# Performance work log

Hardware: AMD Instinct MI355X
Metric: run time of the kernel (lower is better)

Reference implementation:

```python
import jax, jax.numpy as jnp
import numpy as np

N = 1_000_000   # active voxels
C_IN = 32
C_OUT = 32
K = 27          # 3x3x3 kernel volume


def setup_inputs() -> dict:
    key = jax.random.key(0)
    k1, k2, k3, k4, k5 = jax.random.split(key, 5)
    in_feature = jax.random.normal(k1, (N, C_IN), dtype=jnp.float32)
    # torch init: uniform(-std, std), std = 1/sqrt(in_channels * kernel_volume)
    std = 1.0 / np.sqrt(C_IN * K)
    weight = jax.random.uniform(k2, (K, C_IN, C_OUT), jnp.float32, -std, std)
    bias = jax.random.uniform(k3, (C_OUT,), jnp.float32, -std, std)
    # kernel map: for each kernel offset k and each output voxel n, the index of
    # the contributing input voxel, plus a validity mask (sparse neighborhoods)
    kmap_idx = jax.random.randint(k4, (K, N), 0, N, dtype=jnp.int32)
    kmap_valid = jax.random.randint(k5, (K, N), 0, 2, dtype=jnp.int32).astype(bool)
    # center tap of a stride-1 sparse conv always maps voxel to itself
    kmap_idx = kmap_idx.at[K // 2].set(jnp.arange(N, dtype=jnp.int32))
    kmap_valid = kmap_valid.at[K // 2].set(True)
    return {
        "in_feature": in_feature,
        "weight": weight,
        "bias": bias,
        "kmap_idx": kmap_idx,
        "kmap_valid": kmap_valid,
    }


def reference(in_feature, weight, bias, kmap_idx, kmap_valid):
    # Gather-GEMM-scatter sparse conv: out[n] = sum_k W[k]^T @ x[kmap[k,n]] (if valid) + b
    # Loop over the 27 kernel taps (fixed kernel volume) to avoid materializing
    # the full [N, 27, C_in] gathered tensor.
    n_out = kmap_idx.shape[1]
    out = jnp.zeros((n_out, weight.shape[2]), dtype=in_feature.dtype)
    for k in range(weight.shape[0]):
        g = in_feature[kmap_idx[k]] * kmap_valid[k][:, None].astype(in_feature.dtype)
        out = out + jnp.einsum("nc,cd->nd", g, weight[k])
    return out + bias
```

## Files before the change

kernel.cpp:

```cpp
#include <hip/hip_runtime.h>
#include <stdint.h>

#define KVOL 27
#define CIN  32
#define COUT 32

typedef short bf16x8 __attribute__((ext_vector_type(8)));
typedef float f32x4  __attribute__((ext_vector_type(4)));

__global__ void detect_valid_layout(const uint8_t* __restrict__ valid_bytes,
                                    int* __restrict__ flag) {
    __shared__ int s_sum;
    if (threadIdx.x == 0) s_sum = 0;
    __syncthreads();
    int local = 0;
    for (int g = threadIdx.x; g < 1024; g += 256) {
        local += valid_bytes[4 * g + 1] + valid_bytes[4 * g + 2] + valid_bytes[4 * g + 3];
    }
    atomicAdd(&s_sum, local);
    __syncthreads();
    if (threadIdx.x == 0) flag[0] = (s_sum == 0) ? 1 : 0;
}

__device__ inline unsigned short f2bf(float f) {
    unsigned int u = __float_as_uint(f);
    return (unsigned short)((u + 0x7fffu + ((u >> 16) & 1u)) >> 16);
}

__global__ __launch_bounds__(256)
void convert_x(const float* __restrict__ X, short* __restrict__ Xb, int n8) {
    int i = blockIdx.x * blockDim.x + threadIdx.x;
    if (i >= n8) return;
    const float4* p = (const float4*)X + 2 * (size_t)i;
    float4 f0 = p[0], f1 = p[1];
    bf16x8 o;
    o[0] = (short)f2bf(f0.x); o[1] = (short)f2bf(f0.y);
    o[2] = (short)f2bf(f0.z); o[3] = (short)f2bf(f0.w);
    o[4] = (short)f2bf(f1.x); o[5] = (short)f2bf(f1.y);
    o[6] = (short)f2bf(f1.z); o[7] = (short)f2bf(f1.w);
    *((bf16x8*)Xb + (size_t)i) = o;
}

__global__ __launch_bounds__(256)
void convert_w(const float* __restrict__ W, short* __restrict__ Wt) {
    int i = blockIdx.x * blockDim.x + threadIdx.x;
    if (i >= KVOL * CIN * COUT) return;
    int k  = i >> 10;
    int co = (i >> 5) & 31;
    int ci = i & 31;
    Wt[i] = (short)f2bf(W[k * 1024 + ci * 32 + co]);
}

__global__ __launch_bounds__(256)
void sparse_conv_mfma(const short* __restrict__ Xb,
                      const short* __restrict__ Wt,
                      const float* __restrict__ bias,
                      const int* __restrict__ idx,
                      const uint8_t* __restrict__ validb,
                      const int* __restrict__ flag,
                      float* __restrict__ out, int N) {
    const int lane = threadIdx.x & 63;
    const int wave = threadIdx.x >> 6;
    const int col  = lane & 15;
    const int quad = lane >> 4;
    const int base = blockIdx.x * 256 + wave * 64;

    const bool int_layout = (flag[0] != 0);
    const int* validi = (const int*)validb;

    f32x4 acc[4][2] = {};
    const bf16x8 zero = {};

    for (int k = 0; k < KVOL; ++k) {
        const size_t koff = (size_t)k * (size_t)N;
        const bf16x8 b0 = *(const bf16x8*)(Wt + ((k * 32 + col)      * 32 + quad * 8));
        const bf16x8 b1 = *(const bf16x8*)(Wt + ((k * 32 + col + 16) * 32 + quad * 8));
        bf16x8 a[4];
#pragma unroll
        for (int g = 0; g < 4; ++g) {
            const int r = base + g * 16 + col;
            bool v = false;
            int  j = 0;
            if (r < N) {
                v = int_layout ? (validi[koff + r] != 0) : (validb[koff + r] != 0);
                j = idx[koff + r];
            }
            if (v) a[g] = *(const bf16x8*)(Xb + (size_t)j * CIN + quad * 8);
            else   a[g] = zero;
        }
#pragma unroll
        for (int g = 0; g < 4; ++g) {
            acc[g][0] = __builtin_amdgcn_mfma_f32_16x16x32_bf16(a[g], b0, acc[g][0], 0, 0, 0);
            acc[g][1] = __builtin_amdgcn_mfma_f32_16x16x32_bf16(a[g], b1, acc[g][1], 0, 0, 0);
        }
    }

    const float bv0 = bias[col];
    const float bv1 = bias[col + 16];
#pragma unroll
    for (int g = 0; g < 4; ++g) {
#pragma unroll
        for (int r = 0; r < 4; ++r) {
            const int row = base + g * 16 + quad * 4 + r;
            if (row < N) {
                out[(size_t)row * COUT + col]      = acc[g][0][r] + bv0;
                out[(size_t)row * COUT + col + 16] = acc[g][1][r] + bv1;
            }
        }
    }
}

__global__ __launch_bounds__(256)
void sparse_conv_fp32(const float* __restrict__ X,
                      const float* __restrict__ W,
                      const float* __restrict__ B,
                      const int* __restrict__ idx,
                      const uint8_t* __restrict__ validb,
                      const int* __restrict__ flag,
                      float* __restrict__ out,
                      int N) {
    const int n = blockIdx.x * blockDim.x + threadIdx.x;
    if (n >= N) return;
    const bool int_layout = (flag[0] != 0);
    const int* validi = (const int*)validb;
    float acc[COUT];
#pragma unroll
    for (int co = 0; co < COUT; ++co) acc[co] = B[co];
    for (int k = 0; k < KVOL; ++k) {
        const size_t kn = (size_t)k * (size_t)N + (size_t)n;
        const int v = int_layout ? validi[kn] : (int)validb[kn];
        if (v) {
            const int j = idx[kn];
            const float4* xp = (const float4*)(X + (size_t)j * CIN);
            float xr[CIN];
#pragma unroll
            for (int q = 0; q < 8; ++q) {
                float4 t = xp[q];
                xr[4 * q + 0] = t.x; xr[4 * q + 1] = t.y;
                xr[4 * q + 2] = t.z; xr[4 * q + 3] = t.w;
            }
            const float* __restrict__ Wk = W + k * CIN * COUT;
#pragma unroll
            for (int ci = 0; ci < CIN; ++ci) {
                const float xv = xr[ci];
#pragma unroll
                for (int co = 0; co < COUT; ++co) acc[co] += xv * Wk[ci * COUT + co];
            }
        }
    }
    float4* op = (float4*)(out + (size_t)n * COUT);
#pragma unroll
    for (int q = 0; q < 8; ++q)
        op[q] = make_float4(acc[4 * q + 0], acc[4 * q + 1], acc[4 * q + 2], acc[4 * q + 3]);
}

extern "C" void kernel_launch(void* const* d_in, const int* in_sizes, int n_in,
                              void* d_out, int out_size, void* d_ws, size_t ws_size,
                              hipStream_t stream) {
    const float*   X      = (const float*)d_in[0];
    const float*   W      = (const float*)d_in[1];
    const float*   B      = (const float*)d_in[2];
    const int*     idx    = (const int*)d_in[3];
    const uint8_t* validb = (const uint8_t*)d_in[4];

    const int N = in_sizes[0] / CIN;

    const size_t xb_bytes = (size_t)N * CIN * sizeof(short);
    const size_t wt_bytes = (size_t)KVOL * CIN * COUT * sizeof(short);
    const size_t need     = xb_bytes + wt_bytes + 256;

    if (ws_size >= need) {
        short* Xb  = (short*)d_ws;
        short* Wt  = (short*)((char*)d_ws + xb_bytes);
        int*   flag = (int*)((char*)d_ws + xb_bytes + wt_bytes);

        detect_valid_layout<<<1, 256, 0, stream>>>(validb, flag);

        const int n8 = (N * CIN) / 8;
        convert_x<<<(n8 + 255) / 256, 256, 0, stream>>>(X, Xb, n8);
        convert_w<<<(KVOL * CIN * COUT + 255) / 256, 256, 0, stream>>>(W, Wt);

        const int blocks = (N + 255) / 256;
        sparse_conv_mfma<<<blocks, 256, 0, stream>>>(Xb, Wt, B, idx, validb,
                                                     flag, (float*)d_out, N);
    } else {
        int* flag = (int*)d_ws;
        detect_valid_layout<<<1, 256, 0, stream>>>(validb, flag);
        const int blocks = (N + 255) / 256;
        sparse_conv_fp32<<<blocks, 256, 0, stream>>>(X, W, B, idx, validb,
                                                     flag, (float*)d_out, N);
    }
}
```

Measured before the change: 686.2 us.

## Preload kernel map into LDS, use zero sentinel row, double-buffer gathers

Each wave now loads all 27 index/valid pairs for its 64 rows up front in batches of nine, folds validity into the index by pointing invalid entries at an appended zero row of the bf16 feature buffer, and stores the result in shared memory. The tap loop reads indices from LDS and gathers branch-free, alternating two register sets so the next tap's gather is issued before the current tap's MFMAs. This is meant to hide gather latency and remove per-tap scattered index/valid loads and branches. It costs about 27 KB of LDS per block, which may limit occupancy, plus one extra 64-byte row in the workspace.

```diff
diff --git a/kernel.cpp b/kernel.cpp
--- a/kernel.cpp
+++ b/kernel.cpp
@@ -30,6 +30,10 @@
 __global__ __launch_bounds__(256)
 void convert_x(const float* __restrict__ X, short* __restrict__ Xb, int n8) {
     int i = blockIdx.x * blockDim.x + threadIdx.x;
+    if (i < 4) {
+        bf16x8 z = {};
+        *((bf16x8*)Xb + (size_t)n8 + i) = z;
+    }
     if (i >= n8) return;
     const float4* p = (const float4*)X + 2 * (size_t)i;
     float4 f0 = p[0], f1 = p[1];
@@ -65,46 +69,83 @@
     const int quad = lane >> 4;
     const int base = blockIdx.x * 256 + wave * 64;
 
+    __shared__ int s_idx[4][KVOL * 64];
+    int* sw = &s_idx[wave][0];
+
     const bool int_layout = (flag[0] != 0);
     const int* validi = (const int*)validb;
 
+    const int r = base + lane;
+    if (r < N) {
+        if (int_layout) {
+#pragma unroll
+            for (int kc = 0; kc < KVOL; kc += 9) {
+                int j[9], v[9];
+#pragma unroll
+                for (int t = 0; t < 9; ++t) j[t] = idx[(size_t)(kc + t) * N + r];
+#pragma unroll
+                for (int t = 0; t < 9; ++t) v[t] = validi[(size_t)(kc + t) * N + r];
+#pragma unroll
+                for (int t = 0; t < 9; ++t) sw[(kc + t) * 64 + lane] = v[t] ? j[t] : N;
+            }
+        } else {
+#pragma unroll
+            for (int kc = 0; kc < KVOL; kc += 9) {
+                int j[9], v[9];
+#pragma unroll
+                for (int t = 0; t < 9; ++t) j[t] = idx[(size_t)(kc + t) * N + r];
+#pragma unroll
+                for (int t = 0; t < 9; ++t) v[t] = (int)validb[(size_t)(kc + t) * N + r];
+#pragma unroll
+                for (int t = 0; t < 9; ++t) sw[(kc + t) * 64 + lane] = v[t] ? j[t] : N;
+            }
+        }
+    } else {
+#pragma unroll
+        for (int k = 0; k < KVOL; ++k) sw[k * 64 + lane] = N;
+    }
+
     f32x4 acc[4][2] = {};
-    const bf16x8 zero = {};
-
-    for (int k = 0; k < KVOL; ++k) {
-        const size_t koff = (size_t)k * (size_t)N;
-        const bf16x8 b0 = *(const bf16x8*)(Wt + ((k * 32 + col)      * 32 + quad * 8));
-        const bf16x8 b1 = *(const bf16x8*)(Wt + ((k * 32 + col + 16) * 32 + quad * 8));
-        bf16x8 a[4];
+    bf16x8 a0[4], a1[4];
+
+    auto gather = [&](bf16x8 (&a)[4], int k) {
 #pragma unroll
         for (int g = 0; g < 4; ++g) {
-            const int r = base + g * 16 + col;
-            bool v = false;
-            int  j = 0;
-            if (r < N) {
-                v = int_layout ? (validi[koff + r] != 0) : (validb[koff + r] != 0);
-                j = idx[koff + r];
-            }
-            if (v) a[g] = *(const bf16x8*)(Xb + (size_t)j * CIN + quad * 8);
-            else   a[g] = zero;
-        }
+            const int j = sw[k * 64 + g * 16 + col];
+            a[g] = *(const bf16x8*)(Xb + (size_t)j * CIN + quad * 8);
+        }
+    };
+    auto tap = [&](bf16x8 (&a)[4], int k) {
+        const bf16x8 b0 = *(const bf16x8*)(Wt + (k * 1024 + col * 32 + quad * 8));
+        const bf16x8 b1 = *(const bf16x8*)(Wt + (k * 1024 + (col + 16) * 32 + quad * 8));
 #pragma unroll
         for (int g = 0; g < 4; ++g) {
             acc[g][0] = __builtin_amdgcn_mfma_f32_16x16x32_bf16(a[g], b0, acc[g][0], 0, 0, 0);
             acc[g][1] = __builtin_amdgcn_mfma_f32_16x16x32_bf16(a[g], b1, acc[g][1], 0, 0, 0);
         }
-    }
+    };
+
+    gather(a0, 0);
+#pragma unroll 1
+    for (int kk = 0; kk < (KVOL - 1) / 2; ++kk) {
+        const int k = kk * 2;
+        gather(a1, k + 1);
+        tap(a0, k);
+        gather(a0, k + 2);
+        tap(a1, k + 1);
+    }
+    tap(a0, KVOL - 1);
 
     const float bv0 = bias[col];
     const float bv1 = bias[col + 16];
 #pragma unroll
     for (int g = 0; g < 4; ++g) {
 #pragma unroll
-        for (int r = 0; r < 4; ++r) {
-            const int row = base + g * 16 + quad * 4 + r;
+        for (int rr = 0; rr < 4; ++rr) {
+            const int row = base + g * 16 + quad * 4 + rr;
             if (row < N) {
-                out[(size_t)row * COUT + col]      = acc[g][0][r] + bv0;
-                out[(size_t)row * COUT + col + 16] = acc[g][1][r] + bv1;
+                out[(size_t)row * COUT + col]      = acc[g][0][rr] + bv0;
+                out[(size_t)row * COUT + col + 16] = acc[g][1][rr] + bv1;
             }
         }
     }
@@ -165,7 +206,7 @@
 
     const int N = in_sizes[0] / CIN;
 
-    const size_t xb_bytes = (size_t)N * CIN * sizeof(short);
+    const size_t xb_bytes = (size_t)(N + 1) * CIN * sizeof(short);
     const size_t wt_bytes = (size_t)KVOL * CIN * COUT * sizeof(short);
     const size_t need     = xb_bytes + wt_bytes + 256;
 
```

Result: faster. 576.3 us (-16.0%).

## Software-pipeline kmap and gather loads three taps ahead with branchless zero row

Applied to the files above, without the earlier changes.

Restructures the tap loop into a three-stage software pipeline: index/valid loads run several taps ahead and the feature gathers run one stage ahead of the MFMAs. Invalid taps now read a zero row appended to the bf16 feature buffer, so the per-lane branch goes away. Index and valid loads use nontemporal hints, and output stores are nontemporal. The aim is to hide gather latency and cut divergence, at the cost of more registers, which could lower occupancy.

```diff
diff --git a/kernel.cpp b/kernel.cpp
--- a/kernel.cpp
+++ b/kernel.cpp
@@ -30,6 +30,10 @@
 __global__ __launch_bounds__(256)
 void convert_x(const float* __restrict__ X, short* __restrict__ Xb, int n8) {
     int i = blockIdx.x * blockDim.x + threadIdx.x;
+    if (i < 4) {
+        bf16x8 z = {};
+        *((bf16x8*)Xb + (size_t)n8 + i) = z;
+    }
     if (i >= n8) return;
     const float4* p = (const float4*)X + 2 * (size_t)i;
     float4 f0 = p[0], f1 = p[1];
@@ -50,6 +54,8 @@
     int ci = i & 31;
     Wt[i] = (short)f2bf(W[k * 1024 + ci * 32 + co]);
 }
+
+struct JV4 { int j[4]; int v[4]; };
 
 __global__ __launch_bounds__(256)
 void sparse_conv_mfma(const short* __restrict__ Xb,
@@ -65,46 +71,92 @@
     const int quad = lane >> 4;
     const int base = blockIdx.x * 256 + wave * 64;
 
-    const bool int_layout = (flag[0] != 0);
-    const int* validi = (const int*)validb;
+    const int vshift = (flag[0] != 0) ? 2 : 0;
+    const char* XbB = (const char*)Xb;
+    const size_t Nsz = (size_t)N;
+    const unsigned zoff = (unsigned)N << 6;
+
+    int rc[4], ok[4];
+#pragma unroll
+    for (int g = 0; g < 4; ++g) {
+        const int r = base + g * 16 + col;
+        ok[g] = (r < N) ? 1 : 0;
+        rc[g] = (r < N) ? r : (N - 1);
+    }
 
     f32x4 acc[4][2] = {};
-    const bf16x8 zero = {};
-
-    for (int k = 0; k < KVOL; ++k) {
-        const size_t koff = (size_t)k * (size_t)N;
-        const bf16x8 b0 = *(const bf16x8*)(Wt + ((k * 32 + col)      * 32 + quad * 8));
-        const bf16x8 b1 = *(const bf16x8*)(Wt + ((k * 32 + col + 16) * 32 + quad * 8));
-        bf16x8 a[4];
-#pragma unroll
-        for (int g = 0; g < 4; ++g) {
-            const int r = base + g * 16 + col;
-            bool v = false;
-            int  j = 0;
-            if (r < N) {
-                v = int_layout ? (validi[koff + r] != 0) : (validb[koff + r] != 0);
-                j = idx[koff + r];
-            }
-            if (v) a[g] = *(const bf16x8*)(Xb + (size_t)j * CIN + quad * 8);
-            else   a[g] = zero;
-        }
-#pragma unroll
-        for (int g = 0; g < 4; ++g) {
-            acc[g][0] = __builtin_amdgcn_mfma_f32_16x16x32_bf16(a[g], b0, acc[g][0], 0, 0, 0);
-            acc[g][1] = __builtin_amdgcn_mfma_f32_16x16x32_bf16(a[g], b1, acc[g][1], 0, 0, 0);
-        }
-    }
+    bf16x8 a0[4], a1[4], a2[4];
+    JV4 jv0, jv1, jv2;
+
+#define JVLOAD(S, t)                                                          \
+    do {                                                                      \
+        if ((t) < KVOL) {                                                     \
+            const size_t ko = (size_t)(t) * Nsz;                              \
+            _Pragma("unroll") for (int g = 0; g < 4; ++g) {                   \
+                S.j[g] = __builtin_nontemporal_load(idx + ko + rc[g]);        \
+                S.v[g] = (int)__builtin_nontemporal_load(                     \
+                    validb + ((ko + (size_t)rc[g]) << vshift));               \
+            }                                                                 \
+        }                                                                     \
+    } while (0)
+
+#define GI(S, A, t)                                                           \
+    do {                                                                      \
+        if ((t) < KVOL) {                                                     \
+            _Pragma("unroll") for (int g = 0; g < 4; ++g) {                   \
+                const unsigned mm = (ok[g] & (S.v[g] != 0))                   \
+                                        ? ((unsigned)S.j[g] << 6)             \
+                                        : zoff;                               \
+                A[g] = *(const bf16x8*)(XbB + (size_t)mm + quad * 16);        \
+            }                                                                 \
+        }                                                                     \
+    } while (0)
+
+#define TAP(A, t)                                                             \
+    do {                                                                      \
+        if ((t) < KVOL) {                                                     \
+            const bf16x8 b0 =                                                 \
+                *(const bf16x8*)(Wt + ((t) * 1024 + col * 32 + quad * 8));    \
+            const bf16x8 b1 =                                                 \
+                *(const bf16x8*)(Wt +                                         \
+                                 ((t) * 1024 + (col + 16) * 32 + quad * 8));  \
+            _Pragma("unroll") for (int g = 0; g < 4; ++g) {                   \
+                acc[g][0] = __builtin_amdgcn_mfma_f32_16x16x32_bf16(          \
+                    A[g], b0, acc[g][0], 0, 0, 0);                            \
+                acc[g][1] = __builtin_amdgcn_mfma_f32_16x16x32_bf16(          \
+                    A[g], b1, acc[g][1], 0, 0, 0);                            \
+            }                                                                 \
+        }                                                                     \
+    } while (0)
+
+    JVLOAD(jv0, 0); JVLOAD(jv1, 1); JVLOAD(jv2, 2);
+    GI(jv0, a0, 0); JVLOAD(jv0, 3);
+    GI(jv1, a1, 1); JVLOAD(jv1, 4);
+    GI(jv2, a2, 2); JVLOAD(jv2, 5);
+
+#pragma unroll
+    for (int tb = 0; tb < KVOL; tb += 3) {
+        TAP(a0, tb + 0); GI(jv0, a0, tb + 3); JVLOAD(jv0, tb + 6);
+        TAP(a1, tb + 1); GI(jv1, a1, tb + 4); JVLOAD(jv1, tb + 7);
+        TAP(a2, tb + 2); GI(jv2, a2, tb + 5); JVLOAD(jv2, tb + 8);
+    }
+
+#undef JVLOAD
+#undef GI
+#undef TAP
 
     const float bv0 = bias[col];
     const float bv1 = bias[col + 16];
 #pragma unroll
     for (int g = 0; g < 4; ++g) {
 #pragma unroll
-        for (int r = 0; r < 4; ++r) {
-            const int row = base + g * 16 + quad * 4 + r;
+        for (int rr = 0; rr < 4; ++rr) {
+            const int row = base + g * 16 + quad * 4 + rr;
             if (row < N) {
-                out[(size_t)row * COUT + col]      = acc[g][0][r] + bv0;
-                out[(size_t)row * COUT + col + 16] = acc[g][1][r] + bv1;
+                __builtin_nontemporal_store(acc[g][0][rr] + bv0,
+                                            &out[(size_t)row * COUT + col]);
+                __builtin_nontemporal_store(acc[g][1][rr] + bv1,
+                                            &out[(size_t)row * COUT + col + 16]);
             }
         }
     }
@@ -165,7 +217,7 @@
 
     const int N = in_sizes[0] / CIN;
 
-    const size_t xb_bytes = (size_t)N * CIN * sizeof(short);
+    const size_t xb_bytes = (size_t)(N + 1) * CIN * sizeof(short);
     const size_t wt_bytes = (size_t)KVOL * CIN * COUT * sizeof(short);
     const size_t need     = xb_bytes + wt_bytes + 256;
 
```

Result: faster. 587.2 us (-14.4%).
